# Performance work log

Measured on AMD Instinct MI355X. Metric: run time of the kernel, lower is better.

Reference implementation:

```python
import jax, jax.numpy as jnp
import numpy as np

NUM_BANDS = 30
SPLIT_FREQ = 30
M_PARAM = 1
DIM = 2048
BATCH = 16384


def _dct_mat(N):
    # Orthonormal DCT-II matrix D: dct(x) = x @ D.T, idct(y) = y @ D
    n = np.arange(N, dtype=np.float64)
    kk = n[:, None]
    M = np.cos(np.pi * (n + 0.5) * kk / N)
    s = np.full(N, np.sqrt(2.0 / N))
    s[0] = np.sqrt(1.0 / N)
    return jnp.asarray((M * s[:, None]).astype(np.float32))


def _band_scale(freq_weights, k, N):
    # Precompute the per-frequency scale vector the torch loop applies band-by-band.
    pts = np.linspace(0, N - 1, NUM_BANDS + 1).astype(np.int64)  # torch .long() truncation
    scale = jnp.ones((N,), dtype=freq_weights.dtype)
    for i in range(NUM_BANDS):
        s, e = int(pts[i]), int(pts[i + 1])
        if e <= SPLIT_FREQ:
            f = 1.0 + freq_weights[i] * k * (1.0 - i / NUM_BANDS)
        else:
            f = 1.0 - freq_weights[i] * k * (1.0 - (i - NUM_BANDS // M_PARAM) / NUM_BANDS)
        scale = scale.at[s:e].set(f)  # bands are disjoint; base is 1
    return scale


def setup_inputs() -> dict:
    key = jax.random.key(0)
    ks = jax.random.split(key, 6)
    g = 0.02  # small init like xavier_uniform with gain 0.5
    return {
        "x": jax.random.normal(ks[0], (BATCH, DIM), dtype=jnp.float32),
        "freq_weights": jnp.ones((NUM_BANDS,), dtype=jnp.float32),
        "k": jnp.float32(0.3),
        "W1": jax.random.normal(ks[1], (1024, DIM), dtype=jnp.float32) * g,
        "b1": jnp.zeros((1024,), dtype=jnp.float32),
        "W2": jax.random.normal(ks[2], (512, 1024), dtype=jnp.float32) * g,
        "b2": jnp.zeros((512,), dtype=jnp.float32),
        "Wmu": jax.random.normal(ks[3], (256, 512), dtype=jnp.float32) * g,
        "bmu": jnp.zeros((256,), dtype=jnp.float32),
        "Wlv": jax.random.normal(ks[4], (256, 512), dtype=jnp.float32) * g,
        "blv": jnp.zeros((256,), dtype=jnp.float32),
    }


def reference(x, freq_weights, k, W1, b1, W2, b2, Wmu, bmu, Wlv, blv):
    N = x.shape[-1]
    D = _dct_mat(N)
    # DCT -> per-band reweight -> IDCT, fused as two matmuls and one vector multiply
    xd = (x @ D.T) * _band_scale(freq_weights, k, N)
    xe = xd @ D
    h = jax.nn.relu(xe @ W1.T + b1)
    h = jax.nn.relu(h @ W2.T + b2)
    mu = h @ Wmu.T + bmu
    logvar = h @ Wlv.T + blv
    return (mu, logvar)
```

## Files before the change

kernel.cpp:

```cpp
#include <hip/hip_runtime.h>
#include <hip/hip_bf16.h>
#include <math.h>

#define DIM 2048
#define BATCH 16384

typedef __attribute__((ext_vector_type(8))) short short8;
typedef __attribute__((ext_vector_type(4))) short short4v;
typedef __attribute__((ext_vector_type(4))) float floatx4;
typedef unsigned short ushort_t;

__device__ __forceinline__ ushort_t f2bf(float f) {
    union { float f; unsigned u; } v; v.f = f;
    unsigned r = v.u + 0x7FFFu + ((v.u >> 16) & 1u);
    return (ushort_t)(r >> 16);
}

__global__ void k_scale(const float* __restrict__ fw, const float* __restrict__ kp,
                        float* __restrict__ s) {
    int n = blockIdx.x * blockDim.x + threadIdx.x;
    if (n >= DIM) return;
    float kv = kp[0];
    float f = 1.0f;
    for (int i = 0; i < 30; ++i) {
        long s0 = (long)((double)i       * (double)(DIM - 1) / 30.0);
        long e0 = (long)((double)(i + 1) * (double)(DIM - 1) / 30.0);
        if (n >= s0 && n < e0) {
            if (e0 <= 30)
                f = 1.0f + fw[i] * kv * (1.0f - (float)i / 30.0f);
            else
                f = 1.0f - fw[i] * kv * (1.0f - (float)(i - 30) / 30.0f);
        }
    }
    s[n] = f;
}

__global__ void k_gen_d(ushort_t* __restrict__ D, ushort_t* __restrict__ Dt) {
    int idx = blockIdx.x * blockDim.x + threadIdx.x;
    int r = idx >> 11;
    int c = idx & (DIM - 1);
    const float w  = 7.6699039394282058e-4f;
    const float s0 = 0.02209708691207961f;
    const float s1 = 0.03125f;
    int m1 = ((2 * c + 1) * r) & (4 * DIM - 1);
    int m2 = ((2 * r + 1) * c) & (4 * DIM - 1);
    float v1 = __cosf(w * (float)m1) * (r == 0 ? s0 : s1);
    float v2 = __cosf(w * (float)m2) * (c == 0 ? s0 : s1);
    D[idx]  = f2bf(v1);
    Dt[idx] = f2bf(v2);
}

#define U_W1   262144
#define U_W2    65536
#define U_WH    16384
__global__ void k_cast_w(const float* __restrict__ W1, const float* __restrict__ W2,
                         const float* __restrict__ Wmu, const float* __restrict__ Wlv,
                         ushort_t* __restrict__ W1bf, ushort_t* __restrict__ W2bf,
                         ushort_t* __restrict__ Wcat) {
    int i = blockIdx.x * blockDim.x + threadIdx.x;
    const float* src; ushort_t* dst; int u;
    if (i < U_W1)                    { src = W1;  dst = W1bf;             u = i; }
    else if (i < U_W1 + U_W2)        { src = W2;  dst = W2bf;             u = i - U_W1; }
    else if (i < U_W1 + U_W2 + U_WH) { src = Wmu; dst = Wcat;             u = i - U_W1 - U_W2; }
    else                             { src = Wlv; dst = Wcat + 8 * U_WH;  u = i - U_W1 - U_W2 - U_WH; }
    const float4* p = reinterpret_cast<const float4*>(src) + 2 * (size_t)u;
    float4 a = p[0], b = p[1];
    short8 r;
    r[0] = (short)f2bf(a.x); r[1] = (short)f2bf(a.y);
    r[2] = (short)f2bf(a.z); r[3] = (short)f2bf(a.w);
    r[4] = (short)f2bf(b.x); r[5] = (short)f2bf(b.y);
    r[6] = (short)f2bf(b.z); r[7] = (short)f2bf(b.w);
    *reinterpret_cast<short8*>(dst + 8 * (size_t)u) = r;
}

__global__ void k_cast_x(const float* __restrict__ in, ushort_t* __restrict__ out) {
    int i = blockIdx.x * blockDim.x + threadIdx.x;
    const float4* p = reinterpret_cast<const float4*>(in) + 2 * (size_t)i;
    float4 a = p[0], b = p[1];
    short8 r;
    r[0] = (short)f2bf(a.x); r[1] = (short)f2bf(a.y);
    r[2] = (short)f2bf(a.z); r[3] = (short)f2bf(a.w);
    r[4] = (short)f2bf(b.x); r[5] = (short)f2bf(b.y);
    r[6] = (short)f2bf(b.z); r[7] = (short)f2bf(b.w);
    *reinterpret_cast<short8*>(out + 8 * (size_t)i) = r;
}

__global__ void k_red(const float* __restrict__ P, ushort_t* __restrict__ out,
                      const float* __restrict__ scale, int n4, int n4row) {
    int i = blockIdx.x * blockDim.x + threadIdx.x;
    const float4* p = reinterpret_cast<const float4*>(P);
    float4 a = p[i], b = p[i + n4], c = p[i + 2 * n4], d = p[i + 3 * n4];
    float4 s;
    s.x = a.x + b.x + c.x + d.x;
    s.y = a.y + b.y + c.y + d.y;
    s.z = a.z + b.z + c.z + d.z;
    s.w = a.w + b.w + c.w + d.w;
    if (scale) {
        float4 sc = reinterpret_cast<const float4*>(scale)[i & (n4row - 1)];
        s.x *= sc.x; s.y *= sc.y; s.z *= sc.z; s.w *= sc.w;
    }
    short4v o;
    o[0] = (short)f2bf(s.x); o[1] = (short)f2bf(s.y);
    o[2] = (short)f2bf(s.z); o[3] = (short)f2bf(s.w);
    *reinterpret_cast<short4v*>(out + 4 * (size_t)i) = o;
}

template<int TM, int TN, int BK, int EPI, bool SK4>
__device__ __forceinline__ void gemm_core(
        const ushort_t* __restrict__ A, const ushort_t* __restrict__ B,
        ushort_t* __restrict__ Cb, float* __restrict__ Cf,
        const float* __restrict__ ep0, const float* __restrict__ ep1,
        int M, int N, int K, int KC) {
    constexpr int BM = 32 * TM;
    constexpr int BN = 32 * TN;
    constexpr int SEGS = BK / 8;
    constexpr int RSH  = (BK == 32) ? 1 : 0;
    constexpr int SSH  = (SEGS == 4) ? 2 : 3;
    __shared__ __align__(16) ushort_t As[BM * BK];
    __shared__ __align__(16) ushort_t Bs[BN * BK];

    const int tid  = threadIdx.x;
    const int lane = tid & 63;
    const int wave = tid >> 6;
    const int wm   = wave >> 1;
    const int wn   = wave & 1;
    const int q    = lane >> 4;
    const int l16  = lane & 15;

    const int tilesM = M / BM;
    const int tilesN = N / BN;
    int bid = (int)blockIdx.x;
    int sk = 0;
    if constexpr (SK4) { int nt = tilesM * tilesN; sk = bid / nt; bid = bid % nt; }
    const int xcd = bid & 7;
    const int j   = bid >> 3;
    const int bm  = xcd * (tilesM >> 3) + j / tilesN;
    const int bn  = j % tilesN;

    floatx4 acc[TM][TN];
    #pragma unroll
    for (int i = 0; i < TM; ++i)
        #pragma unroll
        for (int jj = 0; jj < TN; ++jj)
            acc[i][jj] = (floatx4){0.f, 0.f, 0.f, 0.f};

    const long aBase = (long)bm * BM * K + (long)sk * KC;
    const long bBase = (long)bn * BN * K + (long)sk * KC;
    const int  KLOOP = SK4 ? KC : K;

    for (int kt = 0; kt < KLOOP; kt += BK) {
        __syncthreads();
        #pragma unroll
        for (int i = 0; i < BM * BK / 2048; ++i) {
            int idx = tid + i * 256;
            int row = idx >> SSH, seg = idx & (SEGS - 1);
            int gseg = seg ^ ((row >> RSH) & (SEGS - 1));
            const ushort_t* g = A + aBase + (long)row * K + kt + gseg * 8;
            __builtin_amdgcn_global_load_lds(
                (const __attribute__((address_space(1))) void*)g,
                (__attribute__((address_space(3))) void*)(As + idx * 8),
                16, 0, 0);
        }
        #pragma unroll
        for (int i = 0; i < BN * BK / 2048; ++i) {
            int idx = tid + i * 256;
            int row = idx >> SSH, seg = idx & (SEGS - 1);
            int gseg = seg ^ ((row >> RSH) & (SEGS - 1));
            const ushort_t* g = B + bBase + (long)row * K + kt + gseg * 8;
            __builtin_amdgcn_global_load_lds(
                (const __attribute__((address_space(1))) void*)g,
                (__attribute__((address_space(3))) void*)(Bs + idx * 8),
                16, 0, 0);
        }
        __syncthreads();

        #pragma unroll
        for (int ks = 0; ks < BK / 32; ++ks) {
            short8 af[TM], bfr[TN];
            #pragma unroll
            for (int t = 0; t < TM; ++t) {
                int srow = wm * TM * 16 + t * 16 + l16;
                int rseg = (ks * 4 + q) ^ ((srow >> RSH) & (SEGS - 1));
                af[t] = *reinterpret_cast<const short8*>(&As[srow * BK + rseg * 8]);
            }
            #pragma unroll
            for (int t = 0; t < TN; ++t) {
                int srow = wn * TN * 16 + t * 16 + l16;
                int rseg = (ks * 4 + q) ^ ((srow >> RSH) & (SEGS - 1));
                bfr[t] = *reinterpret_cast<const short8*>(&Bs[srow * BK + rseg * 8]);
            }
            #pragma unroll
            for (int i = 0; i < TM; ++i)
                #pragma unroll
                for (int jj = 0; jj < TN; ++jj)
                    acc[i][jj] = __builtin_amdgcn_mfma_f32_16x16x32_bf16(
                        af[i], bfr[jj], acc[i][jj], 0, 0, 0);
        }
    }

    #pragma unroll
    for (int i = 0; i < TM; ++i) {
        #pragma unroll
        for (int jj = 0; jj < TN; ++jj) {
            #pragma unroll
            for (int r = 0; r < 4; ++r) {
                int row = bm * BM + wm * TM * 16 + i * 16 + q * 4 + r;
                int col = bn * BN + wn * TN * 16 + jj * 16 + l16;
                float v = acc[i][jj][r];
                if constexpr (EPI == 2) {
                    v += ep0[col];
                    v = v > 0.f ? v : 0.f;
                    Cb[(long)row * N + col] = f2bf(v);
                } else if constexpr (EPI == 3) {
                    const int half = N >> 1;
                    if (col < half)
                        Cf[(long)row * half + col] = v + ep0[col];
                    else
                        Cf[(long)M * half + (long)row * half + (col - half)] = v + ep1[col - half];
                } else {
                    Cf[(long)sk * M * N + (long)row * N + col] = v;
                }
            }
        }
    }
}


__global__ __launch_bounds__(512, 2) void g2_256(const ushort_t* __restrict__ A,
        const ushort_t* __restrict__ B, ushort_t* __restrict__ Cb,
        const float* __restrict__ bias, int M, int N, int K) {
    constexpr int BM = 256, BN = 256, BK = 32;
    __shared__ __align__(16) ushort_t As[4][BM * BK];
    __shared__ __align__(16) ushort_t Bs[4][BN * BK];

    const int tid  = threadIdx.x;
    const int lane = tid & 63;
    const int wave = tid >> 6;
    const int wm   = wave >> 2;
    const int wn   = wave & 3;
    const int q    = lane >> 4;
    const int l16  = lane & 15;

    const int tilesM = M / BM;
    const int tilesN = N / BN;
    int bid = (int)blockIdx.x;
    const int xcd = bid & 7;
    const int jb  = bid >> 3;
    const int bm  = xcd * (tilesM >> 3) + jb / tilesN;
    const int bn  = jb % tilesN;
    const int NT  = K / BK;

    const long aBase = (long)bm * BM * K;
    const long bBase = (long)bn * BN * K;

    floatx4 acc[8][4];
    #pragma unroll
    for (int i = 0; i < 8; ++i)
        #pragma unroll
        for (int j = 0; j < 4; ++j)
            acc[i][j] = (floatx4){0.f, 0.f, 0.f, 0.f};

#define STAGE_A(t) do { int _sl = (t) & 3;                                          \
        _Pragma("unroll")                                                           \
        for (int _g = 0; _g < 2; ++_g) {                                            \
            int _idx = _g * 512 + tid;                                              \
            int _row = _idx >> 2, _seg = _idx & 3;                                  \
            int _gs = _seg ^ ((_row >> 1) & 3);                                     \
            const ushort_t* _gp = A + aBase + (long)_row * K + (t) * BK + _gs * 8;  \
            __builtin_amdgcn_global_load_lds(                                       \
                (const __attribute__((address_space(1))) void*)_gp,                 \
                (__attribute__((address_space(3))) void*)(&As[_sl][_idx * 8]),      \
                16, 0, 0);                                                          \
        } } while (0)
#define STAGE_B(t) do { int _sl = (t) & 3;                                          \
        _Pragma("unroll")                                                           \
        for (int _g = 0; _g < 2; ++_g) {                                            \
            int _idx = _g * 512 + tid;                                              \
            int _row = _idx >> 2, _seg = _idx & 3;                                  \
            int _gs = _seg ^ ((_row >> 1) & 3);                                     \
            const ushort_t* _gp = B + bBase + (long)_row * K + (t) * BK + _gs * 8;  \
            __builtin_amdgcn_global_load_lds(                                       \
                (const __attribute__((address_space(1))) void*)_gp,                 \
                (__attribute__((address_space(3))) void*)(&Bs[_sl][_idx * 8]),      \
                16, 0, 0);                                                          \
        } } while (0)

    STAGE_A(0); STAGE_B(0);
    STAGE_A(1); STAGE_B(1);
    STAGE_A(2); STAGE_B(2);
    asm volatile("s_waitcnt vmcnt(8)" ::: "memory");
    __builtin_amdgcn_s_barrier();
    asm volatile("" ::: "memory");

#define KTILE(tt, DOSTAGE, WAITOP) do {                                             \
        const int _slot = (tt) & 3;                                                 \
        short8 _bf[4], _alo[4], _ahi[4];                                            \
        _Pragma("unroll")                                                           \
        for (int _j = 0; _j < 4; ++_j) {                                            \
            int _sr = wn * 64 + _j * 16 + l16;                                      \
            int _rs = q ^ ((_sr >> 1) & 3);                                         \
            _bf[_j] = *reinterpret_cast<const short8*>(&Bs[_slot][_sr * BK + _rs * 8]); \
        }                                                                           \
        _Pragma("unroll")                                                           \
        for (int _i = 0; _i < 4; ++_i) {                                            \
            int _sr = wm * 128 + _i * 16 + l16;                                     \
            int _rs = q ^ ((_sr >> 1) & 3);                                         \
            _alo[_i] = *reinterpret_cast<const short8*>(&As[_slot][_sr * BK + _rs * 8]); \
        }                                                                           \
        _Pragma("unroll")                                                           \
        for (int _i = 0; _i < 4; ++_i) {                                            \
            int _sr = wm * 128 + 64 + _i * 16 + l16;                                \
            int _rs = q ^ ((_sr >> 1) & 3);                                         \
            _ahi[_i] = *reinterpret_cast<const short8*>(&As[_slot][_sr * BK + _rs * 8]); \
        }                                                                           \
        if (DOSTAGE) { STAGE_A((tt) + 3); STAGE_B((tt) + 3); }                      \
        __builtin_amdgcn_s_setprio(1);                                              \
        _Pragma("unroll")                                                           \
        for (int _i = 0; _i < 4; ++_i)                                              \
            _Pragma("unroll")                                                       \
            for (int _j = 0; _j < 4; ++_j)                                          \
                acc[_i][_j] = __builtin_amdgcn_mfma_f32_16x16x32_bf16(              \
                    _alo[_i], _bf[_j], acc[_i][_j], 0, 0, 0);                       \
        _Pragma("unroll")                                                           \
        for (int _i = 0; _i < 4; ++_i)                                              \
            _Pragma("unroll")                                                       \
            for (int _j = 0; _j < 4; ++_j)                                          \
                acc[4 + _i][_j] = __builtin_amdgcn_mfma_f32_16x16x32_bf16(          \
                    _ahi[_i], _bf[_j], acc[4 + _i][_j], 0, 0, 0);                   \
        __builtin_amdgcn_s_setprio(0);                                              \
        asm volatile("s_waitcnt lgkmcnt(0)" ::: "memory");                          \
        __builtin_amdgcn_sched_barrier(0);                                          \
        WAITOP;                                                                     \
        __builtin_amdgcn_s_barrier();                                               \
        asm volatile("" ::: "memory");                                              \
    } while (0)

    int t = 0;
    for (; t < NT - 3; ++t) {
        KTILE(t, true, asm volatile("s_waitcnt vmcnt(8)" ::: "memory"));
    }
    KTILE(t, false, asm volatile("s_waitcnt vmcnt(4)" ::: "memory")); ++t;
    KTILE(t, false, asm volatile("s_waitcnt vmcnt(0)" ::: "memory")); ++t;
    KTILE(t, false, (void)0);

#undef KTILE
#undef STAGE_A
#undef STAGE_B

    float bsv[4];
    #pragma unroll
    for (int j = 0; j < 4; ++j)
        bsv[j] = bias[bn * BN + wn * 64 + j * 16 + l16];
    #pragma unroll
    for (int i = 0; i < 8; ++i) {
        int row = bm * BM + wm * 128 + i * 16 + q * 4;
        #pragma unroll
        for (int j = 0; j < 4; ++j) {
            int col = bn * BN + wn * 64 + j * 16 + l16;
            #pragma unroll
            for (int r = 0; r < 4; ++r) {
                float v = acc[i][j][r] + bsv[j];
                v = v > 0.f ? v : 0.f;
                Cb[(long)(row + r) * N + col] = f2bf(v);
            }
        }
    }
}

template<int EPI>
__device__ __forceinline__ void gemm128_v2(
        const ushort_t* __restrict__ A, const ushort_t* __restrict__ B,
        ushort_t* __restrict__ Cb, float* __restrict__ Cf,
        const float* __restrict__ ep0, const float* __restrict__ ep1,
        int M, int N, int K) {
    constexpr int BM = 128, BN = 128, BK = 32;
    __shared__ __align__(16) ushort_t As[4][BM * BK];
    __shared__ __align__(16) ushort_t Bs[4][BN * BK];

    const int tid  = threadIdx.x;
    const int lane = tid & 63;
    const int wave = tid >> 6;
    const int wm   = wave >> 1;
    const int wn   = wave & 1;
    const int q    = lane >> 4;
    const int l16  = lane & 15;

    const int tilesM = M / BM;
    const int tilesN = N / BN;
    int bid = (int)blockIdx.x;
    const int xcd = bid & 7;
    const int jb  = bid >> 3;
    const int bm  = xcd * (tilesM >> 3) + jb / tilesN;
    const int bn  = jb % tilesN;
    const int NT  = K / BK;

    const long aBase = (long)bm * BM * K;
    const long bBase = (long)bn * BN * K;

    floatx4 acc[4][4];
    #pragma unroll
    for (int i = 0; i < 4; ++i)
        #pragma unroll
        for (int j = 0; j < 4; ++j)
            acc[i][j] = (floatx4){0.f, 0.f, 0.f, 0.f};

#define STAGE_A(t) do { int _sl = (t) & 3;                                          \
        _Pragma("unroll")                                                           \
        for (int _g = 0; _g < 2; ++_g) {                                            \
            int _idx = _g * 256 + tid;                                              \
            int _row = _idx >> 2, _seg = _idx & 3;                                  \
            int _gs = _seg ^ ((_row >> 1) & 3);                                     \
            const ushort_t* _gp = A + aBase + (long)_row * K + (t) * BK + _gs * 8;  \
            __builtin_amdgcn_global_load_lds(                                       \
                (const __attribute__((address_space(1))) void*)_gp,                 \
                (__attribute__((address_space(3))) void*)(&As[_sl][_idx * 8]),      \
                16, 0, 0);                                                          \
        } } while (0)
#define STAGE_B(t) do { int _sl = (t) & 3;                                          \
        _Pragma("unroll")                                                           \
        for (int _g = 0; _g < 2; ++_g) {                                            \
            int _idx = _g * 256 + tid;                                              \
            int _row = _idx >> 2, _seg = _idx & 3;                                  \
            int _gs = _seg ^ ((_row >> 1) & 3);                                     \
            const ushort_t* _gp = B + bBase + (long)_row * K + (t) * BK + _gs * 8;  \
            __builtin_amdgcn_global_load_lds(                                       \
                (const __attribute__((address_space(1))) void*)_gp,                 \
                (__attribute__((address_space(3))) void*)(&Bs[_sl][_idx * 8]),      \
                16, 0, 0);                                                          \
        } } while (0)

    STAGE_A(0); STAGE_B(0);
    STAGE_A(1); STAGE_B(1);
    STAGE_A(2); STAGE_B(2);
    asm volatile("s_waitcnt vmcnt(8)" ::: "memory");
    __builtin_amdgcn_s_barrier();
    asm volatile("" ::: "memory");

#define KTILE(tt, DOSTAGE, WAITOP) do {                                             \
        const int _slot = (tt) & 3;                                                 \
        short8 _bf[4], _af[4];                                                      \
        _Pragma("unroll")                                                           \
        for (int _j = 0; _j < 4; ++_j) {                                            \
            int _sr = wn * 64 + _j * 16 + l16;                                      \
            int _rs = q ^ ((_sr >> 1) & 3);                                         \
            _bf[_j] = *reinterpret_cast<const short8*>(&Bs[_slot][_sr * BK + _rs * 8]); \
        }                                                                           \
        _Pragma("unroll")                                                           \
        for (int _i = 0; _i < 4; ++_i) {                                            \
            int _sr = wm * 64 + _i * 16 + l16;                                      \
            int _rs = q ^ ((_sr >> 1) & 3);                                         \
            _af[_i] = *reinterpret_cast<const short8*>(&As[_slot][_sr * BK + _rs * 8]); \
        }                                                                           \
        if (DOSTAGE) { STAGE_A((tt) + 3); STAGE_B((tt) + 3); }                      \
        __builtin_amdgcn_s_setprio(1);                                              \
        _Pragma("unroll")                                                           \
        for (int _i = 0; _i < 4; ++_i)                                              \
            _Pragma("unroll")                                                       \
            for (int _j = 0; _j < 4; ++_j)                                          \
                acc[_i][_j] = __builtin_amdgcn_mfma_f32_16x16x32_bf16(              \
                    _af[_i], _bf[_j], acc[_i][_j], 0, 0, 0);                        \
        __builtin_amdgcn_s_setprio(0);                                              \
        asm volatile("s_waitcnt lgkmcnt(0)" ::: "memory");                          \
        __builtin_amdgcn_sched_barrier(0);                                          \
        WAITOP;                                                                     \
        __builtin_amdgcn_s_barrier();                                               \
        asm volatile("" ::: "memory");                                              \
    } while (0)

    int t = 0;
    for (; t < NT - 3; ++t) {
        KTILE(t, true, asm volatile("s_waitcnt vmcnt(8)" ::: "memory"));
    }
    KTILE(t, false, asm volatile("s_waitcnt vmcnt(4)" ::: "memory")); ++t;
    KTILE(t, false, asm volatile("s_waitcnt vmcnt(0)" ::: "memory")); ++t;
    KTILE(t, false, (void)0);

#undef KTILE
#undef STAGE_A
#undef STAGE_B

    #pragma unroll
    for (int i = 0; i < 4; ++i) {
        #pragma unroll
        for (int jj = 0; jj < 4; ++jj) {
            #pragma unroll
            for (int r = 0; r < 4; ++r) {
                int row = bm * BM + wm * 64 + i * 16 + q * 4 + r;
                int col = bn * BN + wn * 64 + jj * 16 + l16;
                float v = acc[i][jj][r];
                if constexpr (EPI == 2) {
                    v += ep0[col];
                    v = v > 0.f ? v : 0.f;
                    Cb[(long)row * N + col] = f2bf(v);
                } else {
                    const int half = N >> 1;
                    v += (col < half) ? ep0[col] : ep1[col - half];
                    if (col < half)
                        Cf[(long)row * half + col] = v;
                    else
                        Cf[(long)M * half + (long)row * half + (col - half)] = v;
                }
            }
        }
    }
}

__global__ __launch_bounds__(256) void g0p_sk(const ushort_t* A, const ushort_t* B,
        float* P, int M, int N, int K, int KC) {
    gemm_core<4, 4, 32, 4, true>(A, B, nullptr, P, nullptr, nullptr, M, N, K, KC);
}
__global__ __launch_bounds__(256) void g1p_sk(const ushort_t* A, const ushort_t* B,
        float* P, int M, int N, int K, int KC) {
    gemm_core<4, 4, 32, 4, true>(A, B, nullptr, P, nullptr, nullptr, M, N, K, KC);
}
__global__ __launch_bounds__(256, 2) void g3_h2(const ushort_t* A, const ushort_t* B,
        ushort_t* Cb, const float* ep0, int M, int N, int K) {
    gemm128_v2<2>(A, B, Cb, nullptr, ep0, nullptr, M, N, K);
}
__global__ __launch_bounds__(256, 2) void g4_head(const ushort_t* A, const ushort_t* B,
        float* Cf, const float* ep0, const float* ep1, int M, int N, int K) {
    gemm128_v2<3>(A, B, nullptr, Cf, ep0, ep1, M, N, K);
}

extern "C" void kernel_launch(void* const* d_in, const int* in_sizes, int n_in,
                              void* d_out, int out_size, void* d_ws, size_t ws_size,
                              hipStream_t stream) {
    const float* x   = (const float*)d_in[0];
    const float* fw  = (const float*)d_in[1];
    const float* kp  = (const float*)d_in[2];
    const float* W1  = (const float*)d_in[3];
    const float* b1  = (const float*)d_in[4];
    const float* W2  = (const float*)d_in[5];
    const float* b2  = (const float*)d_in[6];
    const float* Wmu = (const float*)d_in[7];
    const float* bmu = (const float*)d_in[8];
    const float* Wlv = (const float*)d_in[9];
    const float* blv = (const float*)d_in[10];
    float* out = (float*)d_out;

    char* ws = (char*)d_ws;
    const size_t MB = 1024 * 1024;
    ushort_t* W1bf = (ushort_t*)(ws + 0);
    ushort_t* Dbf  = (ushort_t*)(ws + 4   * MB);
    ushort_t* Dtbf = (ushort_t*)(ws + 12  * MB);
    ushort_t* T1sT = (ushort_t*)(ws + 20  * MB);
    ushort_t* H1   = (ushort_t*)(ws + 0);
    float*    P    = (float*)   (ws + 32  * MB);
    ushort_t* Xbf  = (ushort_t*)(ws + 32  * MB);
    ushort_t* H2   = (ushort_t*)(ws + 96  * MB);
    ushort_t* M1T  = (ushort_t*)(ws + 112 * MB);
    ushort_t* W2bf = (ushort_t*)(ws + 116 * MB);
    ushort_t* Wcat = (ushort_t*)(ws + 117 * MB);
    float*    svec = (float*)   (ws + 118 * MB);

    hipLaunchKernelGGL(k_scale, dim3(DIM / 256), dim3(256), 0, stream, fw, kp, svec);
    hipLaunchKernelGGL(k_gen_d, dim3(DIM * DIM / 256), dim3(256), 0, stream, Dbf, Dtbf);
    hipLaunchKernelGGL(k_cast_w, dim3((U_W1 + U_W2 + 2 * U_WH) / 256), dim3(256), 0, stream,
                       W1, W2, Wmu, Wlv, W1bf, W2bf, Wcat);

    hipLaunchKernelGGL(g0p_sk, dim3(8 * 16 * 4), dim3(256), 0, stream,
                       W1bf, Dbf, P, 1024, 2048, 2048, 512);
    hipLaunchKernelGGL(k_red, dim3(1024 * 2048 / 4 / 256), dim3(256), 0, stream,
                       P, T1sT, svec, 1024 * 2048 / 4, 2048 / 4);
    hipLaunchKernelGGL(g1p_sk, dim3(8 * 16 * 4), dim3(256), 0, stream,
                       T1sT, Dtbf, P, 1024, 2048, 2048, 512);
    hipLaunchKernelGGL(k_red, dim3(1024 * 2048 / 4 / 256), dim3(256), 0, stream,
                       P, M1T, nullptr, 1024 * 2048 / 4, 2048 / 4);

    hipLaunchKernelGGL(k_cast_x, dim3(BATCH * DIM / 8 / 256), dim3(256), 0, stream, x, Xbf);

    hipLaunchKernelGGL(g2_256, dim3((BATCH / 256) * (1024 / 256)), dim3(512), 0, stream,
                       Xbf, M1T, H1, b1, BATCH, 1024, 2048);
    hipLaunchKernelGGL(g3_h2, dim3((BATCH / 128) * (512 / 128)), dim3(256), 0, stream,
                       H1, W2bf, H2, b2, BATCH, 512, 1024);
    hipLaunchKernelGGL(g4_head, dim3((BATCH / 128) * (512 / 128)), dim3(256), 0, stream,
                       H2, Wcat, out, bmu, blv, BATCH, 512, 512);

    (void)in_sizes; (void)n_in; (void)out_size; (void)ws_size;
}
```

Measured before the change: 377.3 us.

## Fuse fp32-to-bf16 cast of x into the first GEMM's A-tile loading

```diff
diff --git a/kernel.cpp b/kernel.cpp
--- a/kernel.cpp
+++ b/kernel.cpp
@@ -73,18 +73,6 @@
     *reinterpret_cast<short8*>(dst + 8 * (size_t)u) = r;
 }
 
-__global__ void k_cast_x(const float* __restrict__ in, ushort_t* __restrict__ out) {
-    int i = blockIdx.x * blockDim.x + threadIdx.x;
-    const float4* p = reinterpret_cast<const float4*>(in) + 2 * (size_t)i;
-    float4 a = p[0], b = p[1];
-    short8 r;
-    r[0] = (short)f2bf(a.x); r[1] = (short)f2bf(a.y);
-    r[2] = (short)f2bf(a.z); r[3] = (short)f2bf(a.w);
-    r[4] = (short)f2bf(b.x); r[5] = (short)f2bf(b.y);
-    r[6] = (short)f2bf(b.z); r[7] = (short)f2bf(b.w);
-    *reinterpret_cast<short8*>(out + 8 * (size_t)i) = r;
-}
-
 __global__ void k_red(const float* __restrict__ P, ushort_t* __restrict__ out,
                       const float* __restrict__ scale, int n4, int n4row) {
     int i = blockIdx.x * blockDim.x + threadIdx.x;
@@ -225,8 +213,7 @@
     }
 }
 
-
-__global__ __launch_bounds__(512, 2) void g2_256(const ushort_t* __restrict__ A,
+__global__ __launch_bounds__(512, 2) void g2f(const float* __restrict__ Xf,
         const ushort_t* __restrict__ B, ushort_t* __restrict__ Cb,
         const float* __restrict__ bias, int M, int N, int K) {
     constexpr int BM = 256, BN = 256, BK = 32;
@@ -260,40 +247,49 @@
         for (int j = 0; j < 4; ++j)
             acc[i][j] = (floatx4){0.f, 0.f, 0.f, 0.f};
 
-#define STAGE_A(t) do { int _sl = (t) & 3;                                          \
+    float4 rAa[4], rAb[4];
+
+#define LDA(tt, RA) do {                                                            \
         _Pragma("unroll")                                                           \
         for (int _g = 0; _g < 2; ++_g) {                                            \
             int _idx = _g * 512 + tid;                                              \
             int _row = _idx >> 2, _seg = _idx & 3;                                  \
             int _gs = _seg ^ ((_row >> 1) & 3);                                     \
-            const ushort_t* _gp = A + aBase + (long)_row * K + (t) * BK + _gs * 8;  \
-            __builtin_amdgcn_global_load_lds(                                       \
-                (const __attribute__((address_space(1))) void*)_gp,                 \
-                (__attribute__((address_space(3))) void*)(&As[_sl][_idx * 8]),      \
-                16, 0, 0);                                                          \
+            const float4* _p = reinterpret_cast<const float4*>(                     \
+                Xf + aBase + (long)_row * K + (tt) * BK + _gs * 8);                 \
+            RA[2 * _g]     = _p[0];                                                 \
+            RA[2 * _g + 1] = _p[1];                                                 \
         } } while (0)
-#define STAGE_B(t) do { int _sl = (t) & 3;                                          \
+
+#define CVW(tt, RA) do { const int _sl = (tt) & 3;                                  \
+        _Pragma("unroll")                                                           \
+        for (int _g = 0; _g < 2; ++_g) {                                            \
+            int _idx = _g * 512 + tid;                                              \
+            float4 _a = RA[2 * _g], _b = RA[2 * _g + 1];                            \
+            short8 _o;                                                              \
+            _o[0] = (short)f2bf(_a.x); _o[1] = (short)f2bf(_a.y);                   \
+            _o[2] = (short)f2bf(_a.z); _o[3] = (short)f2bf(_a.w);                   \
+            _o[4] = (short)f2bf(_b.x); _o[5] = (short)f2bf(_b.y);                   \
+            _o[6] = (short)f2bf(_b.z); _o[7] = (short)f2bf(_b.w);                   \
+            *reinterpret_cast<short8*>(&As[_sl][_idx * 8]) = _o;                    \
+        } } while (0)
+
+#define STG_B(tt) do { const int _sl = (tt) & 3;                                    \
         _Pragma("unroll")                                                           \
         for (int _g = 0; _g < 2; ++_g) {                                            \
             int _idx = _g * 512 + tid;                                              \
             int _row = _idx >> 2, _seg = _idx & 3;                                  \
             int _gs = _seg ^ ((_row >> 1) & 3);                                     \
-            const ushort_t* _gp = B + bBase + (long)_row * K + (t) * BK + _gs * 8;  \
+            const ushort_t* _gp = B + bBase + (long)_row * K + (tt) * BK + _gs * 8; \
             __builtin_amdgcn_global_load_lds(                                       \
                 (const __attribute__((address_space(1))) void*)_gp,                 \
                 (__attribute__((address_space(3))) void*)(&Bs[_sl][_idx * 8]),      \
                 16, 0, 0);                                                          \
         } } while (0)
 
-    STAGE_A(0); STAGE_B(0);
-    STAGE_A(1); STAGE_B(1);
-    STAGE_A(2); STAGE_B(2);
-    asm volatile("s_waitcnt vmcnt(8)" ::: "memory");
-    __builtin_amdgcn_s_barrier();
-    asm volatile("" ::: "memory");
-
-#define KTILE(tt, DOSTAGE, WAITOP) do {                                             \
+#define ITER(tt, RA) do {                                                           \
         const int _slot = (tt) & 3;                                                 \
+        if ((tt) + 2 < NT) CVW((tt) + 2, RA);                                       \
         short8 _bf[4], _alo[4], _ahi[4];                                            \
         _Pragma("unroll")                                                           \
         for (int _j = 0; _j < 4; ++_j) {                                            \
@@ -313,7 +309,8 @@
             int _rs = q ^ ((_sr >> 1) & 3);                                         \
             _ahi[_i] = *reinterpret_cast<const short8*>(&As[_slot][_sr * BK + _rs * 8]); \
         }                                                                           \
-        if (DOSTAGE) { STAGE_A((tt) + 3); STAGE_B((tt) + 3); }                      \
+        if ((tt) + 3 < NT) STG_B((tt) + 3);                                         \
+        if ((tt) + 4 < NT) LDA((tt) + 4, RA);                                       \
         __builtin_amdgcn_s_setprio(1);                                              \
         _Pragma("unroll")                                                           \
         for (int _i = 0; _i < 4; ++_i)                                              \
@@ -330,22 +327,30 @@
         __builtin_amdgcn_s_setprio(0);                                              \
         asm volatile("s_waitcnt lgkmcnt(0)" ::: "memory");                          \
         __builtin_amdgcn_sched_barrier(0);                                          \
-        WAITOP;                                                                     \
+        if ((tt) == NT - 2)                                                         \
+            asm volatile("s_waitcnt vmcnt(0)" ::: "memory");                        \
         __builtin_amdgcn_s_barrier();                                               \
         asm volatile("" ::: "memory");                                              \
     } while (0)
 
-    int t = 0;
-    for (; t < NT - 3; ++t) {
-        KTILE(t, true, asm volatile("s_waitcnt vmcnt(8)" ::: "memory"));
-    }
-    KTILE(t, false, asm volatile("s_waitcnt vmcnt(4)" ::: "memory")); ++t;
-    KTILE(t, false, asm volatile("s_waitcnt vmcnt(0)" ::: "memory")); ++t;
-    KTILE(t, false, (void)0);
-
-#undef KTILE
-#undef STAGE_A
-#undef STAGE_B
+    LDA(0, rAa); CVW(0, rAa);
+    LDA(1, rAb); CVW(1, rAb);
+    LDA(2, rAa); LDA(3, rAb);
+    STG_B(0); STG_B(1); STG_B(2);
+    asm volatile("s_waitcnt lgkmcnt(0)" ::: "memory");
+    asm volatile("s_waitcnt vmcnt(4)" ::: "memory");
+    __builtin_amdgcn_s_barrier();
+    asm volatile("" ::: "memory");
+
+    for (int t = 0; t < NT; t += 2) {
+        ITER(t, rAa);
+        ITER(t + 1, rAb);
+    }
+
+#undef ITER
+#undef STG_B
+#undef CVW
+#undef LDA
 
     float bsv[4];
     #pragma unroll
@@ -546,7 +551,6 @@
     ushort_t* T1sT = (ushort_t*)(ws + 20  * MB);
     ushort_t* H1   = (ushort_t*)(ws + 0);
     float*    P    = (float*)   (ws + 32  * MB);
-    ushort_t* Xbf  = (ushort_t*)(ws + 32  * MB);
     ushort_t* H2   = (ushort_t*)(ws + 96  * MB);
     ushort_t* M1T  = (ushort_t*)(ws + 112 * MB);
     ushort_t* W2bf = (ushort_t*)(ws + 116 * MB);
@@ -567,10 +571,8 @@
     hipLaunchKernelGGL(k_red, dim3(1024 * 2048 / 4 / 256), dim3(256), 0, stream,
                        P, M1T, nullptr, 1024 * 2048 / 4, 2048 / 4);
 
-    hipLaunchKernelGGL(k_cast_x, dim3(BATCH * DIM / 8 / 256), dim3(256), 0, stream, x, Xbf);
-
-    hipLaunchKernelGGL(g2_256, dim3((BATCH / 256) * (1024 / 256)), dim3(512), 0, stream,
-                       Xbf, M1T, H1, b1, BATCH, 1024, 2048);
+    hipLaunchKernelGGL(g2f, dim3((BATCH / 256) * (1024 / 256)), dim3(512), 0, stream,
+                       x, M1T, H1, b1, BATCH, 1024, 2048);
     hipLaunchKernelGGL(g3_h2, dim3((BATCH / 128) * (512 / 128)), dim3(256), 0, stream,
                        H1, W2bf, H2, b2, BATCH, 512, 1024);
     hipLaunchKernelGGL(g4_head, dim3((BATCH / 128) * (512 / 128)), dim3(256), 0, stream,
```

New measurement: 376.6 us. No clear change (-0.2%).
